# Optimization experiments

Hardware: AMD Instinct MI355X
Metric: run time of the kernel (lower is better)

## Reference

```python
import math
import jax, jax.numpy as jnp
import numpy as np

COULOMB = 14.399645478425668  # eV*Angstrom / e^2


def setup_inputs() -> dict:
    key = jax.random.key(0)
    k0, k1, k2, k3, k4 = jax.random.split(key, 5)
    B, n, F, S = 128, 512, 64, 4  # molecules, atoms/molecule, feat dim, n species
    N = B * n
    node_features = jax.random.normal(k0, (N, F), dtype=jnp.float32)
    pos = jax.random.normal(k1, (N, 3), dtype=jnp.float32) * 5.0  # spread atoms out
    atom_type = jax.random.randint(k2, (N,), 0, S)
    total_charge = jnp.zeros((B, 1), dtype=jnp.float32)
    chi_weight = jax.random.normal(k3, (F, 1), dtype=jnp.float32) / np.float32(np.sqrt(F))
    hardness_param = jnp.ones((S,), dtype=jnp.float32)
    sigma = 0.3 + 0.5 * jax.random.uniform(k4, (S,), dtype=jnp.float32)  # covalent radii
    return dict(node_features=node_features, pos=pos, atom_type=atom_type,
                total_charge=total_charge, chi_weight=chi_weight,
                hardness_param=hardness_param, sigma=sigma, n_per_mol=n)


def reference(node_features, pos, atom_type, total_charge, chi_weight,
              hardness_param, sigma, n_per_mol):
    n = n_per_mol
    N, F = node_features.shape
    B = N // n

    feats = node_features.reshape(B, n, F)
    pos_b = pos.reshape(B, n, 3)
    sp = atom_type.reshape(B, n)

    chi = (feats @ chi_weight)[..., 0]                      # [B, n] electronegativity
    hard = jnp.square(hardness_param)[sp]                   # [B, n]
    sig = sigma[sp]                                         # [B, n]

    # pairwise distances within each molecule (diag masked for safe divide)
    diff = pos_b[:, :, None, :] - pos_b[:, None, :, :]      # [B, n, n, 3]
    d2 = jnp.sum(diff * diff, axis=-1)
    eye = jnp.eye(n, dtype=pos.dtype)
    d = jnp.sqrt(jnp.where(eye, 1.0, d2))                   # [B, n, n]

    gamma = jnp.sqrt(sig[:, :, None] ** 2 + sig[:, None, :] ** 2)
    off = COULOMB * jax.lax.erf(d / (math.sqrt(2.0) * gamma)) / d
    diag = hard + COULOMB / (math.sqrt(math.pi) * sig)      # [B, n]
    coeffs = off * (1.0 - eye) + eye * diag[:, :, None]     # [B, n, n]

    # augmented Qeq system with charge-conservation Lagrange multiplier
    A = jnp.ones((B, n + 1, n + 1), dtype=coeffs.dtype)
    A = A.at[:, :n, :n].set(coeffs)
    A = A.at[:, n, n].set(0.0)
    rhs = jnp.concatenate([-chi, total_charge], axis=1)     # [B, n+1]
    sol = jnp.linalg.solve(A, rhs[..., None])[..., 0]
    q = sol[:, :n]                                          # [B, n] charges

    # E = sum_{i<j} C_ij q_i q_j + sum_i (chi_i q_i + 0.5 diag_i q_i^2)
    #   = 0.5 q^T C q + chi . q   (C includes diagonal)
    e_qeq = 0.5 * jnp.einsum('bi,bij,bj->b', q, coeffs, q) + jnp.sum(chi * q, axis=1)
    return e_qeq[:, None], q.reshape(N, 1)
```

## Files before the change

kernel.cpp:

```cpp
#include <hip/hip_runtime.h>
#include <math.h>

#define NA 512
#define NN (NA*NA)
#define COULOMB 14.399645478425668f
#define SQRT_PI 1.7724538509055160273f

#define TB 320
#define TS 192
#define TSTR 193

typedef float v2f __attribute__((ext_vector_type(2)));

__device__ __forceinline__ float rl(float x, int lane) {
    return __int_as_float(__builtin_amdgcn_readlane(__float_as_int(x), lane));
}

__device__ __forceinline__ float pair_val(float dx, float dy, float dz,
                                          float s2i, float s2k) {
    float d2 = dx*dx + dy*dy + dz*dz;
    float rinv = rsqrtf(d2);
    return COULOMB * erff(d2 * rinv * rsqrtf(2.f * (s2i + s2k))) * rinv;
}

__global__ void k_pre(const float* __restrict__ feats, const float* __restrict__ w,
                      const int* __restrict__ type, const float* __restrict__ hard,
                      const float* __restrict__ sigma,
                      float* __restrict__ chi, float* __restrict__ diag,
                      float* __restrict__ sigA,
                      float* __restrict__ r1, float* __restrict__ r2, int N) {
    __shared__ float wl[64];
    int tid = threadIdx.x;
    if (tid < 64) wl[tid] = w[tid];
    __syncthreads();
    int i = blockIdx.x * 256 + tid;
    if (i >= N) return;
    const float4* fp = (const float4*)(feats + (size_t)i * 64);
    float acc = 0.f;
#pragma unroll
    for (int q = 0; q < 16; q++) {
        float4 v = fp[q];
        acc += v.x * wl[4*q] + v.y * wl[4*q+1] + v.z * wl[4*q+2] + v.w * wl[4*q+3];
    }
    chi[i] = acc;
    r1[i] = acc;
    r2[i] = 1.0f;
    int t = type[i];
    float s = sigma[t];
    float h = hard[t];
    sigA[i] = s;
    diag[i] = h * h + COULOMB / (SQRT_PI * s);
}

__global__ void __launch_bounds__(256, 1) k_panel(const float* __restrict__ pos,
                                                  const float* __restrict__ sigA,
                                                  const float* __restrict__ diagA,
                                                  float* __restrict__ C,
                                                  float* __restrict__ r1,
                                                  float* __restrict__ r2, const int j) {
    const int q = blockIdx.x;
    const int b = blockIdx.y;
    float* __restrict__ Cb = C + (size_t)b * NN;
    const int jb = j * 64;
    const int m = NA - jb - 64;
    const int tid = threadIdx.x;
    __shared__ float D[64 * 65];
    __shared__ float DT[64 * 64];
    __shared__ float invd[64];
    __shared__ float y1s[64], y2s[64];
    __shared__ float px[NA], py[NA], pz[NA], s2s[NA];

    if (j == 0) {
#pragma unroll
        for (int e = 0; e < 2; e++) {
            int i = e * 256 + tid;
            px[i] = pos[((size_t)b * NA + i) * 3 + 0];
            py[i] = pos[((size_t)b * NA + i) * 3 + 1];
            pz[i] = pos[((size_t)b * NA + i) * 3 + 2];
            float s = sigA[b * NA + i];
            s2s[i] = s * s;
        }
        __syncthreads();
    }

#pragma unroll
    for (int e = 0; e < 16; e++) {
        int f = e * 256 + tid;
        int rr = f >> 6, cc = f & 63;
        float v;
        if (j == 0) {
            if (rr == cc) v = diagA[b * NA + rr];
            else v = pair_val(px[rr]-px[cc], py[rr]-py[cc], pz[rr]-pz[cc], s2s[rr], s2s[cc]);
        } else {
            v = Cb[(size_t)(jb + rr) * NA + jb + cc];
        }
        D[rr * 65 + cc] = v;
    }

    const int h = m >> 1;
    const int r0 = q ? h : 0;
    const int nr = q ? (m - h) : h;
    const int r = tid - 32;
    const bool hasrow = (r >= 0 && r < nr);
    const int grow = jb + 64 + r0 + r;
    float rv[64];
    if (hasrow) {
        if (j == 0) {
#pragma unroll
            for (int k = 0; k < 64; k++)
                rv[k] = pair_val(px[grow]-px[k], py[grow]-py[k], pz[grow]-pz[k],
                                 s2s[grow], s2s[k]);
        } else {
            const float4* rp = (const float4*)(Cb + (size_t)grow * NA + jb);
#pragma unroll
            for (int qq = 0; qq < 16; qq++) {
                float4 v = rp[qq];
                rv[4*qq] = v.x; rv[4*qq+1] = v.y; rv[4*qq+2] = v.z; rv[4*qq+3] = v.w;
            }
        }
    }
    __syncthreads();

    if (tid < 64) {
        const int t = tid;
        float cl[64];
#pragma unroll
        for (int i = 0; i < 64; i++) cl[i] = (i >= t) ? D[i * 65 + t] : D[t * 65 + i];
#pragma unroll
        for (int k = 0; k < 64; k++) {
            float pivot = rl(cl[k], k);
            float invp = 1.0f / pivot;
            float factor = (t > k) ? (cl[k] * invp) : 0.0f;
#pragma unroll
            for (int i = k + 1; i < 64; i++) {
                float bc = rl(cl[i], k);
                cl[i] -= bc * factor;
            }
        }
        float rs = 1.0f / sqrtf(cl[t]);
        invd[t] = rs;
#pragma unroll
        for (int i = 0; i < 64; i++)
            if (i >= t) D[i * 65 + t] = cl[i] * rs;

        float v1 = r1[(size_t)b * NA + jb + t];
        float v2 = r2[(size_t)b * NA + jb + t];
#pragma unroll
        for (int k = 0; k < 64; k++) {
            float rsk = rl(rs, k);
            float y1k = rl(v1, k) * rsk;
            float y2k = rl(v2, k) * rsk;
            if (t == k) {
                y1s[t] = y1k; y2s[t] = y2k;
                if (q == 0) {
                    r1[(size_t)b * NA + jb + t] = y1k;
                    r2[(size_t)b * NA + jb + t] = y2k;
                }
            }
            float lv = (t > k) ? D[t * 65 + k] : 0.f;
            v1 -= lv * y1k;
            v2 -= lv * y2k;
        }
    }
    __syncthreads();

#pragma unroll
    for (int e = 0; e < 16; e++) {
        int f = e * 256 + tid;
        int row = f >> 6, cc = f & 63;
        float v = D[row * 65 + cc];
        DT[row * 64 + cc] = (cc < row) ? v : 0.f;
        if (q == 0 && cc <= row) Cb[(size_t)(jb + row) * NA + jb + cc] = v;
    }
    __syncthreads();

    if (hasrow) {
#pragma unroll
        for (int k = 0; k < 64; k++) {
            float acc = rv[k];
            const float4* Lr = (const float4*)(DT + k * 64);
            const int k4 = k >> 2;
#pragma unroll
            for (int t4 = 0; t4 < k4; t4++) {
                float4 Lv = Lr[t4];
                acc -= Lv.x * rv[4*t4] + Lv.y * rv[4*t4+1] + Lv.z * rv[4*t4+2] + Lv.w * rv[4*t4+3];
            }
#pragma unroll
            for (int tt = k4 * 4; tt < k; tt++) acc -= DT[k * 64 + tt] * rv[tt];
            rv[k] = acc * invd[k];
        }
        float4* rp = (float4*)(Cb + (size_t)grow * NA + jb);
#pragma unroll
        for (int qq = 0; qq < 16; qq++)
            rp[qq] = make_float4(rv[4*qq], rv[4*qq+1], rv[4*qq+2], rv[4*qq+3]);

        float a1 = 0.f, a2 = 0.f;
#pragma unroll
        for (int k = 0; k < 64; k++) {
            a1 = fmaf(rv[k], y1s[k], a1);
            a2 = fmaf(rv[k], y2s[k], a2);
        }
        r1[(size_t)b * NA + grow] -= a1;
        r2[(size_t)b * NA + grow] -= a2;
    }
}

template<bool GEN>
__global__ void __launch_bounds__(256, 2) k_trail(float* __restrict__ C,
                                                  const float* __restrict__ pos,
                                                  const float* __restrict__ sigA,
                                                  const float* __restrict__ diagA,
                                                  const int j) {
    const int b = blockIdx.y;
    float* __restrict__ Cb = C + (size_t)b * NN;
    const int jb = j * 64;
    const int m = NA - jb - 64;
    int t = blockIdx.x;
    int RI = 0;
    while (t >= RI + 1) { t -= RI + 1; RI++; }
    const int RJ = t;
    const int RB = RI * 128, CB = RJ * 128;
    const int vr = min(128, m - RB);
    const int vc = min(128, m - CB);
    const int tid = threadIdx.x;
    const int rg = tid >> 4, cg = tid & 15;

    __shared__ float As[128 * 66];
    __shared__ float Bs[128 * 66];

    v2f ac2[8][8];

    if (GEN) {
        __shared__ float pAx[128], pAy[128], pAz[128], sA[128], dA[128];
        __shared__ float pBx[128], pBy[128], pBz[128], sB[128];
        if (tid < 128) {
            if (RB + tid < m) {
                int ga = b * NA + jb + 64 + RB + tid;
                pAx[tid] = pos[(size_t)ga * 3 + 0];
                pAy[tid] = pos[(size_t)ga * 3 + 1];
                pAz[tid] = pos[(size_t)ga * 3 + 2];
                float s = sigA[ga]; sA[tid] = s * s;
                dA[tid] = diagA[ga];
            }
        } else {
            int u = tid - 128;
            if (CB + u < m) {
                int gb = b * NA + jb + 64 + CB + u;
                pBx[u] = pos[(size_t)gb * 3 + 0];
                pBy[u] = pos[(size_t)gb * 3 + 1];
                pBz[u] = pos[(size_t)gb * 3 + 2];
                float s = sigA[gb]; sB[u] = s * s;
            }
        }
        __syncthreads();
#pragma unroll
        for (int rr = 0; rr < 8; rr++) {
            int row = rg * 8 + rr;
#pragma unroll
            for (int cc = 0; cc < 8; cc++) {
                int col = cg + 16 * cc;
                float iv;
                if (RB + row == CB + col)
                    iv = dA[row];
                else
                    iv = pair_val(pAx[row]-pBx[col], pAy[row]-pBy[col],
                                  pAz[row]-pBz[col], sA[row], sB[col]);
                ac2[rr][cc].x = iv;
                ac2[rr][cc].y = 0.f;
            }
        }
        __syncthreads();
    } else {
        const int GRB = jb + 64 + RB, GCB = jb + 64 + CB;
#pragma unroll
        for (int rr = 0; rr < 8; rr++) {
            int row = rg * 8 + rr;
#pragma unroll
            for (int cc = 0; cc < 8; cc++) {
                int col = cg + 16 * cc;
                ac2[rr][cc].x = (row < vr && col < vc)
                    ? Cb[(size_t)(GRB + row) * NA + GCB + col] : 0.f;
                ac2[rr][cc].y = 0.f;
            }
        }
    }

    const float* Pan = Cb + (size_t)(jb + 64) * NA + jb;
#pragma unroll
    for (int e = 0; e < 8; e++) {
        int f = e * 256 + tid;
        int row = f >> 4, s = f & 15;
        float4 v = make_float4(0.f, 0.f, 0.f, 0.f);
        if (row < vr) v = *(const float4*)(Pan + (size_t)(RB + row) * NA + s * 4);
        As[row * 66 + s * 4 + 0] = v.x;
        As[row * 66 + s * 4 + 1] = v.y;
        As[row * 66 + s * 4 + 2] = v.z;
        As[row * 66 + s * 4 + 3] = v.w;
        float4 u = make_float4(0.f, 0.f, 0.f, 0.f);
        if (row < vc) u = *(const float4*)(Pan + (size_t)(CB + row) * NA + s * 4);
        Bs[row * 66 + s * 4 + 0] = u.x;
        Bs[row * 66 + s * 4 + 1] = u.y;
        Bs[row * 66 + s * 4 + 2] = u.z;
        Bs[row * 66 + s * 4 + 3] = u.w;
    }
    __syncthreads();

#pragma unroll 2
    for (int k = 0; k < 64; k += 2) {
        v2f ai2[8], bj2[8];
#pragma unroll
        for (int rr = 0; rr < 8; rr++)
            ai2[rr] = *(const v2f*)&As[(rg * 8 + rr) * 66 + k];
#pragma unroll
        for (int cc = 0; cc < 8; cc++)
            bj2[cc] = *(const v2f*)&Bs[(cg + 16 * cc) * 66 + k];
#pragma unroll
        for (int rr = 0; rr < 8; rr++)
#pragma unroll
            for (int cc = 0; cc < 8; cc++) {
                ac2[rr][cc].x = fmaf(-ai2[rr].x, bj2[cc].x, ac2[rr][cc].x);
                ac2[rr][cc].y = fmaf(-ai2[rr].y, bj2[cc].y, ac2[rr][cc].y);
            }
    }

    const int GRB = jb + 64 + RB, GCB = jb + 64 + CB;
#pragma unroll
    for (int rr = 0; rr < 8; rr++) {
        int row = rg * 8 + rr;
        if (row < vr) {
#pragma unroll
            for (int cc = 0; cc < 8; cc++) {
                int col = cg + 16 * cc;
                if (col < vc)
                    Cb[(size_t)(GRB + row) * NA + GCB + col] = ac2[rr][cc].x + ac2[rr][cc].y;
            }
        }
    }
}

__global__ void __launch_bounds__(256, 1) k_tail(float* __restrict__ C,
                                                 float* __restrict__ r1,
                                                 float* __restrict__ r2) {
    const int b = blockIdx.x;
    float* __restrict__ Cb = C + (size_t)b * NN;
    const int tid = threadIdx.x;
    __shared__ float T[TS * TSTR];
    __shared__ float invd[64], y1s[64], y2s[64];

    for (int f = tid; f < TS * TS; f += 256) {
        int row = f / TS, c = f - row * TS;
        T[row * TSTR + c] = Cb[(size_t)(TB + row) * NA + TB + c];
    }
    __syncthreads();

#pragma unroll 1
    for (int p = 0; p < 3; p++) {
        const int pb = p * 64;
        const int msub = TS - pb - 64;

        if (tid < 64) {
            const int t = tid;
            float cl[64];
#pragma unroll
            for (int i = 0; i < 64; i++)
                cl[i] = (i >= t) ? T[(pb + i) * TSTR + pb + t]
                                 : T[(pb + t) * TSTR + pb + i];
#pragma unroll
            for (int k = 0; k < 64; k++) {
                float pivot = rl(cl[k], k);
                float invp = 1.0f / pivot;
                float factor = (t > k) ? (cl[k] * invp) : 0.0f;
#pragma unroll
                for (int i = k + 1; i < 64; i++) {
                    float bc = rl(cl[i], k);
                    cl[i] -= bc * factor;
                }
            }
            float rs = 1.0f / sqrtf(cl[t]);
            invd[t] = rs;
#pragma unroll
            for (int i = 0; i < 64; i++) {
                float lv = cl[i] * rs;
                if (i >= t) T[(pb + i) * TSTR + pb + t] = lv;
                if (i > t)  T[(pb + t) * TSTR + pb + i] = lv;
            }
            float v1 = r1[(size_t)b * NA + TB + pb + t];
            float v2 = r2[(size_t)b * NA + TB + pb + t];
#pragma unroll
            for (int k = 0; k < 64; k++) {
                float rsk = rl(rs, k);
                float y1k = rl(v1, k) * rsk;
                float y2k = rl(v2, k) * rsk;
                if (t == k) {
                    y1s[t] = y1k; y2s[t] = y2k;
                    r1[(size_t)b * NA + TB + pb + t] = y1k;
                    r2[(size_t)b * NA + TB + pb + t] = y2k;
                }
                float lv = (t > k) ? T[(pb + t) * TSTR + pb + k] : 0.f;
                v1 -= lv * y1k;
                v2 -= lv * y2k;
            }
        }
        __syncthreads();

        if (msub > 0) {
            if (tid < msub) {
                const int row_l = pb + 64 + tid;
                float rv[64];
#pragma unroll
                for (int k = 0; k < 64; k++) rv[k] = T[row_l * TSTR + pb + k];
#pragma unroll
                for (int k = 0; k < 64; k++) {
                    float yk = rv[k] * invd[k];
                    rv[k] = yk;
                    const float* LTrow = &T[(pb + k) * TSTR + pb];
#pragma unroll
                    for (int i = k + 1; i < 64; i++)
                        rv[i] -= LTrow[i] * yk;
                }
#pragma unroll
                for (int k = 0; k < 64; k++) T[row_l * TSTR + pb + k] = rv[k];
                float a1 = 0.f, a2 = 0.f;
#pragma unroll
                for (int k = 0; k < 64; k++) {
                    a1 = fmaf(rv[k], y1s[k], a1);
                    a2 = fmaf(rv[k], y2s[k], a2);
                }
                r1[(size_t)b * NA + TB + row_l] -= a1;
                r2[(size_t)b * NA + TB + row_l] -= a2;
            }
            __syncthreads();

            const int rbase = pb + 64;
            if (p == 0) {
                const int rg = tid >> 4, cg = tid & 15;
                float acc[8][8];
#pragma unroll
                for (int rr = 0; rr < 8; rr++)
#pragma unroll
                    for (int cc = 0; cc < 8; cc++)
                        acc[rr][cc] = T[(rbase + rg * 8 + rr) * TSTR + rbase + cg * 8 + cc];
#pragma unroll 4
                for (int k = 0; k < 64; k++) {
                    float ai[8], bj[8];
#pragma unroll
                    for (int rr = 0; rr < 8; rr++)
                        ai[rr] = T[(rbase + rg * 8 + rr) * TSTR + pb + k];
#pragma unroll
                    for (int cc = 0; cc < 8; cc++)
                        bj[cc] = T[(rbase + cg * 8 + cc) * TSTR + pb + k];
#pragma unroll
                    for (int rr = 0; rr < 8; rr++)
#pragma unroll
                        for (int cc = 0; cc < 8; cc++)
                            acc[rr][cc] = fmaf(-ai[rr], bj[cc], acc[rr][cc]);
                }
#pragma unroll
                for (int rr = 0; rr < 8; rr++)
#pragma unroll
                    for (int cc = 0; cc < 8; cc++)
                        T[(rbase + rg * 8 + rr) * TSTR + rbase + cg * 8 + cc] = acc[rr][cc];
            } else {
                const int rg = tid >> 4, cg = tid & 15;
                float acc[4][4];
#pragma unroll
                for (int rr = 0; rr < 4; rr++)
#pragma unroll
                    for (int cc = 0; cc < 4; cc++)
                        acc[rr][cc] = T[(rbase + rg * 4 + rr) * TSTR + rbase + cg * 4 + cc];
#pragma unroll 4
                for (int k = 0; k < 64; k++) {
                    float ai[4], bj[4];
#pragma unroll
                    for (int rr = 0; rr < 4; rr++)
                        ai[rr] = T[(rbase + rg * 4 + rr) * TSTR + pb + k];
#pragma unroll
                    for (int cc = 0; cc < 4; cc++)
                        bj[cc] = T[(rbase + cg * 4 + cc) * TSTR + pb + k];
#pragma unroll
                    for (int rr = 0; rr < 4; rr++)
#pragma unroll
                        for (int cc = 0; cc < 4; cc++)
                            acc[rr][cc] = fmaf(-ai[rr], bj[cc], acc[rr][cc]);
                }
#pragma unroll
                for (int rr = 0; rr < 4; rr++)
#pragma unroll
                    for (int cc = 0; cc < 4; cc++)
                        T[(rbase + rg * 4 + rr) * TSTR + rbase + cg * 4 + cc] = acc[rr][cc];
            }
        }
        __syncthreads();
    }

    for (int f = tid; f < TS * TS; f += 256) {
        int row = f / TS, c = f - row * TS;
        Cb[(size_t)(TB + row) * NA + TB + c] = T[row * TSTR + c];
    }
}

__global__ void __launch_bounds__(512, 1) k_back(const float* __restrict__ C,
                                                 float* __restrict__ r1g,
                                                 float* __restrict__ r2g) {
    const int b = blockIdx.x;
    const int rhs = blockIdx.y;
    const float* Cb = C + (size_t)b * NN;
    const int tid = threadIdx.x;
    __shared__ float D[64 * 65];
    __shared__ float r[NA];
    __shared__ float pb[4][NA];

    float* rg = rhs ? r2g : r1g;
    r[tid] = rg[(size_t)b * NA + tid];

    const int ii = tid & 127;
    const int gg = tid >> 7;
    for (int j = 7; j >= 0; j--) {
        const int jb = j * 64;
        __syncthreads();
#pragma unroll
        for (int e = 0; e < 8; e++) {
            int f = e * 512 + tid;
            int row = f >> 6, cc = f & 63;
            D[row * 65 + cc] = Cb[(size_t)(jb + row) * NA + jb + cc];
        }
        __syncthreads();
        if (tid < 64) {
            float val = r[jb + tid];
            float idg = 1.0f / D[tid * 65 + tid];
#pragma unroll
            for (int k = 63; k >= 0; k--) {
                float xk = rl(val, k) * rl(idg, k);
                if (tid == k) r[jb + k] = xk;
                float lv = (tid < k) ? D[k * 65 + tid] : 0.f;
                val -= lv * xk;
            }
        }
        __syncthreads();
        if (jb > 0) {
            const int nf4 = jb >> 2;
            float4 s1 = make_float4(0.f, 0.f, 0.f, 0.f);
            if (ii < nf4) {
#pragma unroll
                for (int gq = 0; gq < 16; gq++) {
                    int g = jb + gg * 16 + gq;
                    float x1 = r[g];
                    float4 Lv = *(const float4*)(Cb + (size_t)g * NA + ii * 4);
                    s1.x += Lv.x * x1; s1.y += Lv.y * x1; s1.z += Lv.z * x1; s1.w += Lv.w * x1;
                }
            }
            *(float4*)(&pb[gg][ii * 4]) = s1;
            __syncthreads();
            if (tid < jb)
                r[tid] -= pb[0][tid] + pb[1][tid] + pb[2][tid] + pb[3][tid];
        }
    }
    __syncthreads();

    rg[(size_t)b * NA + tid] = r[tid];
}

__global__ void __launch_bounds__(512, 1) k_final(const float* __restrict__ x1,
                                                  const float* __restrict__ x2,
                                                  const float* __restrict__ chiA,
                                                  const float* __restrict__ Qtot,
                                                  float* __restrict__ out, int B) {
    const int b = blockIdx.x;
    const int tid = threadIdx.x;
    __shared__ float red[16];
    __shared__ float muS;

    float v1 = x1[(size_t)b * NA + tid];
    float v2 = x2[(size_t)b * NA + tid];

    float s1p = v1, s2p = v2;
#pragma unroll
    for (int off = 1; off < 64; off <<= 1) {
        s1p += __shfl_xor(s1p, off);
        s2p += __shfl_xor(s2p, off);
    }
    if ((tid & 63) == 0) { red[tid >> 6] = s1p; red[8 + (tid >> 6)] = s2p; }
    __syncthreads();
    if (tid == 0) {
        float s1 = 0.f, s2 = 0.f;
#pragma unroll
        for (int wv = 0; wv < 8; wv++) { s1 += red[wv]; s2 += red[8 + wv]; }
        muS = -(Qtot[b] + s1) / s2;
    }
    __syncthreads();
    float mu = muS;
    float qv = -v1 - mu * v2;
    out[B + (size_t)b * NA + tid] = qv;

    float eacc = chiA[b * NA + tid] * qv;
#pragma unroll
    for (int off = 1; off < 64; off <<= 1) eacc += __shfl_xor(eacc, off);
    __syncthreads();
    if ((tid & 63) == 0) red[tid >> 6] = eacc;
    __syncthreads();
    if (tid == 0) {
        float e = 0.f;
#pragma unroll
        for (int wv = 0; wv < 8; wv++) e += red[wv];
        out[b] = 0.5f * e - 0.5f * mu * Qtot[b];
    }
}

extern "C" void kernel_launch(void* const* d_in, const int* in_sizes, int n_in,
                              void* d_out, int out_size, void* d_ws, size_t ws_size,
                              hipStream_t stream) {
    const int B = in_sizes[3];
    const int N = in_sizes[2];
    const float* feats = (const float*)d_in[0];
    const float* pos   = (const float*)d_in[1];
    const int*   type  = (const int*)d_in[2];
    const float* Qt    = (const float*)d_in[3];
    const float* w     = (const float*)d_in[4];
    const float* hard  = (const float*)d_in[5];
    const float* sig   = (const float*)d_in[6];
    float* out = (float*)d_out;
    float* ws  = (float*)d_ws;

    float* C    = ws;
    float* chi  = ws + (size_t)B * NN;
    float* diag = chi + N;
    float* sigA = diag + N;
    float* r1   = sigA + N;
    float* r2   = r1 + N;

    k_pre<<<(N + 255) / 256, 256, 0, stream>>>(feats, w, type, hard, sig,
                                               chi, diag, sigA, r1, r2, N);

    static const int tilesJ[5] = {10, 6, 6, 3, 3};
    for (int j = 0; j < 5; j++) {
        k_panel<<<dim3(2, B), 256, 0, stream>>>(pos, sigA, diag, C, r1, r2, j);
        if (j == 0)
            k_trail<true><<<dim3(tilesJ[j], B), 256, 0, stream>>>(C, pos, sigA, diag, j);
        else
            k_trail<false><<<dim3(tilesJ[j], B), 256, 0, stream>>>(C, pos, sigA, diag, j);
    }
    k_tail<<<B, 256, 0, stream>>>(C, r1, r2);
    k_back<<<dim3(B, 2), 512, 0, stream>>>(C, r1, r2);
    k_final<<<B, 512, 0, stream>>>(r1, r2, chi, Qt, out, B);
}
```

Before: 725.5 us.

## Invert diagonal Cholesky block and spread panel TRSM across all threads

In the tail factorization, the first wavefront now builds the explicit inverse of each 64x64 diagonal Cholesky block with cross-lane readlane operations and stores it in the block's upper triangle. The panel triangular solve then becomes a multiply by that inverse, split by column across all 256 threads instead of one serial forward-substitution chain per row on only msub threads. This targets the long dependent FMA chains and idle threads of the old solve. In exchange, the inverse costs roughly 2k readlanes on one wave, uses extra registers, and reads LDS with float4 at addresses that may be misaligned because the row stride is 193.

```diff
diff --git a/kernel.cpp b/kernel.cpp
--- a/kernel.cpp
+++ b/kernel.cpp
@@ -338,6 +338,36 @@
     }
 }
 
+template<int S, int NQ, int PART>
+__device__ __forceinline__ void trsm_rows(float* __restrict__ T,
+                                          const float* __restrict__ invd,
+                                          const int pb, const int row_l) {
+    float rv[64];
+    const float* Ar = &T[row_l * TSTR + pb];
+#pragma unroll
+    for (int k4 = 0; k4 < 16; k4++) {
+        float4 v = *(const float4*)(Ar + 4 * k4);
+        rv[4*k4+0] = v.x; rv[4*k4+1] = v.y; rv[4*k4+2] = v.z; rv[4*k4+3] = v.w;
+    }
+    float x[NQ];
+#pragma unroll
+    for (int q = 0; q < NQ; q++) x[q] = 0.f;
+#pragma unroll
+    for (int k = 0; k < 64; k++) {
+        const float a = rv[k];
+        const float* Mrow = &T[(pb + k) * TSTR + pb];
+#pragma unroll
+        for (int q = 0; q < NQ; q++) {
+            const int i = PART + S * q;
+            if (i > k)       x[q] = fmaf(a, Mrow[i], x[q]);
+            else if (i == k) x[q] = fmaf(a, invd[k], x[q]);
+        }
+    }
+#pragma unroll
+    for (int q = 0; q < NQ; q++)
+        T[row_l * TSTR + pb + PART + S * q] = x[q];
+}
+
 __global__ void __launch_bounds__(256, 1) k_tail(float* __restrict__ C,
                                                  float* __restrict__ r1,
                                                  float* __restrict__ r2) {
@@ -378,12 +408,31 @@
             }
             float rs = 1.0f / sqrtf(cl[t]);
             invd[t] = rs;
-#pragma unroll
-            for (int i = 0; i < 64; i++) {
-                float lv = cl[i] * rs;
-                if (i >= t) T[(pb + i) * TSTR + pb + t] = lv;
-                if (i > t)  T[(pb + t) * TSTR + pb + i] = lv;
-            }
+            float ls[64];
+#pragma unroll
+            for (int i = 0; i < 64; i++) ls[i] = cl[i] * rs;
+#pragma unroll
+            for (int i = 0; i < 64; i++)
+                if (i >= t) T[(pb + i) * TSTR + pb + t] = ls[i];
+
+            if (p < 2) {
+                float m[64];
+#pragma unroll
+                for (int i = 0; i < 64; i++) m[i] = (i == t) ? rs : 0.f;
+#pragma unroll
+                for (int k = 1; k < 64; k++) {
+                    float acc = 0.f;
+#pragma unroll
+                    for (int jj = 0; jj < k; jj++)
+                        acc += rl(ls[k], jj) * m[jj];
+                    float mk = -rl(rs, k) * acc;
+                    if (t < k) m[k] = mk;
+                }
+#pragma unroll
+                for (int k = 0; k < 64; k++)
+                    if (k > t) T[(pb + t) * TSTR + pb + k] = m[k];
+            }
+
             float v1 = r1[(size_t)b * NA + TB + pb + t];
             float v2 = r2[(size_t)b * NA + TB + pb + t];
 #pragma unroll
@@ -404,32 +453,32 @@
         __syncthreads();
 
         if (msub > 0) {
+            if (p == 0) {
+                const int row_l = pb + 64 + (tid & 127);
+                if ((tid >> 7) == 0) trsm_rows<2, 32, 0>(T, invd, pb, row_l);
+                else                 trsm_rows<2, 32, 1>(T, invd, pb, row_l);
+            } else {
+                const int row_l = pb + 64 + (tid & 63);
+                const int part = tid >> 6;
+                if      (part == 0) trsm_rows<4, 16, 0>(T, invd, pb, row_l);
+                else if (part == 1) trsm_rows<4, 16, 1>(T, invd, pb, row_l);
+                else if (part == 2) trsm_rows<4, 16, 2>(T, invd, pb, row_l);
+                else                trsm_rows<4, 16, 3>(T, invd, pb, row_l);
+            }
+            __syncthreads();
+
             if (tid < msub) {
                 const int row_l = pb + 64 + tid;
-                float rv[64];
-#pragma unroll
-                for (int k = 0; k < 64; k++) rv[k] = T[row_l * TSTR + pb + k];
+                float a1 = 0.f, a2 = 0.f;
 #pragma unroll
                 for (int k = 0; k < 64; k++) {
-                    float yk = rv[k] * invd[k];
-                    rv[k] = yk;
-                    const float* LTrow = &T[(pb + k) * TSTR + pb];
-#pragma unroll
-                    for (int i = k + 1; i < 64; i++)
-                        rv[i] -= LTrow[i] * yk;
-                }
-#pragma unroll
-                for (int k = 0; k < 64; k++) T[row_l * TSTR + pb + k] = rv[k];
-                float a1 = 0.f, a2 = 0.f;
-#pragma unroll
-                for (int k = 0; k < 64; k++) {
-                    a1 = fmaf(rv[k], y1s[k], a1);
-                    a2 = fmaf(rv[k], y2s[k], a2);
+                    float xv = T[row_l * TSTR + pb + k];
+                    a1 = fmaf(xv, y1s[k], a1);
+                    a2 = fmaf(xv, y2s[k], a2);
                 }
                 r1[(size_t)b * NA + TB + row_l] -= a1;
                 r2[(size_t)b * NA + TB + row_l] -= a2;
             }
-            __syncthreads();
 
             const int rbase = pb + 64;
             if (p == 0) {
```

Measured after the change: 806.0 us. +11.1%, slower.
